# Kernel optimization log

Hardware: AMD Instinct MI355X
Metric: run time of the kernel (lower is better)

## Reference

```python
import jax, jax.numpy as jnp
import numpy as np

EMBED_DIM = 1024
BATCH, SEQ = 4, 2048


def setup_inputs() -> dict:
    key = jax.random.key(0)
    kx, kq, kk, kv = jax.random.split(key, 4)
    return {
        "x": jax.random.normal(kx, (BATCH, SEQ, EMBED_DIM), dtype=jnp.float32),
        "q_weight": jax.random.normal(kq, (EMBED_DIM, EMBED_DIM), dtype=jnp.float32),
        "k_weight": jax.random.normal(kk, (EMBED_DIM, EMBED_DIM), dtype=jnp.float32),
        "v_weight": jax.random.normal(kv, (EMBED_DIM, EMBED_DIM), dtype=jnp.float32),
    }


def reference(x, q_weight, k_weight, v_weight):
    # x: [b, s, d]
    d = x.shape[-1]
    Q = jnp.einsum('bsd,de->bse', x, q_weight)
    K = jnp.einsum('bsd,de->bse', x, k_weight)
    V = jnp.einsum('bsd,de->bse', x, v_weight)
    scores = jnp.einsum('bqe,bke->bqk', Q, K) / jnp.sqrt(jnp.float32(d))
    attn = jax.nn.softmax(scores, axis=-1)
    out = jnp.einsum('bqk,bke->bqe', attn, V)
    return out
```

## Files before the change

### kernel.cpp

```cpp
#include <hip/hip_runtime.h>
#include <hip/hip_bf16.h>


typedef _Float16 half8 __attribute__((ext_vector_type(8)));
typedef _Float16 half4v __attribute__((ext_vector_type(4)));
typedef float f32x16 __attribute__((ext_vector_type(16)));
typedef float f32x4 __attribute__((ext_vector_type(4)));

#define GLOBAL_AS __attribute__((address_space(1)))
#define LDS_AS __attribute__((address_space(3)))

__device__ __forceinline__ void gll16(const _Float16* g, _Float16* l) {
    __builtin_amdgcn_global_load_lds((GLOBAL_AS const void*)g, (LDS_AS void*)l, 16, 0, 0);
}

__device__ __forceinline__ void lgkm0_pin() {
    asm volatile("s_waitcnt lgkmcnt(0)" ::: "memory");
    __builtin_amdgcn_sched_barrier(0);
}

__device__ __forceinline__ void barrier_fence() {
    asm volatile("s_barrier" ::: "memory");
}

__device__ __forceinline__ void vmwait0() {
    asm volatile("s_waitcnt vmcnt(0)" ::: "memory");
}

__device__ __forceinline__ void vmwait4() {
    asm volatile("s_waitcnt vmcnt(4)" ::: "memory");
}

template <int NPROD, int OUTMODE>
__global__ __launch_bounds__(256) void gemm_nt(
    const _Float16* __restrict__ A0, const _Float16* __restrict__ A1,
    const _Float16* __restrict__ B0, const _Float16* __restrict__ B1,
    float* __restrict__ Cf, _Float16* __restrict__ C0, _Float16* __restrict__ C1,
    int lda, int ldb, int ldc, int K,
    long sA, long sB, long sC, float scale, float scale2) {
    constexpr int NTILES = (NPROD == 3) ? 4 : 2;
    constexpr int BUFH = NTILES * 4096;
    __shared__ alignas(16) _Float16 smem[2 * BUFH];

    const int tid = threadIdx.x;
    const int wave = tid >> 6, lane = tid & 63;
    const int wm = (wave >> 1) * 64, wn = (wave & 1) * 64;
    const int q2 = lane >> 5, r32 = lane & 31;

    const long zA = (long)blockIdx.z * sA;
    const long zB = (long)blockIdx.z * sB;
    const long zC = (long)blockIdx.z * sC;

    const float sc = (blockIdx.y * 2 < gridDim.y) ? scale : scale2;

    const int trow = tid >> 2;
    const int tcol = (((tid & 3) - ((tid >> 3) & 3) - ((tid >> 6) & 3)) & 3) * 8;
    const _Float16* gA0 = A0 + zA + (long)(blockIdx.x * 128 + trow) * lda + tcol;
    const _Float16* gB0 = B0 + zB + (long)(blockIdx.y * 128 + trow) * ldb + tcol;
    const _Float16* gA1 = (NPROD == 3) ? (A1 + zA + (long)(blockIdx.x * 128 + trow) * lda + tcol) : nullptr;
    const _Float16* gB1 = (NPROD == 3) ? (B1 + zB + (long)(blockIdx.y * 128 + trow) * ldb + tcol) : nullptr;

    f32x16 acc[2][2];
#pragma unroll
    for (int i = 0; i < 2; ++i)
#pragma unroll
        for (int j = 0; j < 2; ++j)
#pragma unroll
            for (int r = 0; r < 16; ++r) acc[i][j][r] = 0.f;

    const int ldsoff = tid * 8;
    const int fbase = q2 + (r32 >> 1) + (r32 >> 4);

    {
        _Float16* s = smem;
        gll16(gA0, s + ldsoff);
        gll16(gA0 + 64 * lda, s + ldsoff + 2048);
        gll16(gB0, s + 4096 + ldsoff);
        gll16(gB0 + 64 * ldb, s + 4096 + ldsoff + 2048);
        if (NPROD == 3) {
            gll16(gA1, s + 8192 + ldsoff);
            gll16(gA1 + 64 * lda, s + 8192 + ldsoff + 2048);
            gll16(gB1, s + 12288 + ldsoff);
            gll16(gB1 + 64 * ldb, s + 12288 + ldsoff + 2048);
        }
        gA0 += 32; gB0 += 32;
        if (NPROD == 3) { gA1 += 32; gB1 += 32; }
    }

    int buf = 0;
    for (int k0 = 0; k0 < K; k0 += 32) {
        __syncthreads();

        if (k0 + 32 < K) {
            _Float16* s = smem + (buf ^ 1) * BUFH;
            gll16(gA0, s + ldsoff);
            gll16(gA0 + 64 * lda, s + ldsoff + 2048);
            gll16(gB0, s + 4096 + ldsoff);
            gll16(gB0 + 64 * ldb, s + 4096 + ldsoff + 2048);
            if (NPROD == 3) {
                gll16(gA1, s + 8192 + ldsoff);
                gll16(gA1 + 64 * lda, s + 8192 + ldsoff + 2048);
                gll16(gB1, s + 12288 + ldsoff);
                gll16(gB1 + 64 * ldb, s + 12288 + ldsoff + 2048);
            }
            gA0 += 32; gB0 += 32;
            if (NPROD == 3) { gA1 += 32; gB1 += 32; }
        }

        _Float16* sA0 = smem + buf * BUFH;
        _Float16* sB0 = sA0 + 4096;
        _Float16* sA1 = (NPROD == 3) ? sA0 + 8192 : sA0;
        _Float16* sB1 = (NPROD == 3) ? sA0 + 12288 : sA0;
#pragma unroll
        for (int h = 0; h < 2; ++h) {
            half8 a0[2], b0[2], a1[2], b1[2];
#pragma unroll
            for (int i = 0; i < 2; ++i) {
                const int pp = ((fbase + 2 * i + 2 * h) & 3) * 8;
                a0[i] = *(const half8*)(sA0 + (wm + i * 32 + r32) * 32 + pp);
                b0[i] = *(const half8*)(sB0 + (wn + i * 32 + r32) * 32 + pp);
                if (NPROD == 3) {
                    a1[i] = *(const half8*)(sA1 + (wm + i * 32 + r32) * 32 + pp);
                    b1[i] = *(const half8*)(sB1 + (wn + i * 32 + r32) * 32 + pp);
                }
            }
#pragma unroll
            for (int i = 0; i < 2; ++i)
#pragma unroll
                for (int j = 0; j < 2; ++j) {
                    acc[i][j] = __builtin_amdgcn_mfma_f32_32x32x16_f16(a0[i], b0[j], acc[i][j], 0, 0, 0);
                    if (NPROD == 3) {
                        acc[i][j] = __builtin_amdgcn_mfma_f32_32x32x16_f16(a0[i], b1[j], acc[i][j], 0, 0, 0);
                        acc[i][j] = __builtin_amdgcn_mfma_f32_32x32x16_f16(a1[i], b0[j], acc[i][j], 0, 0, 0);
                    }
                }
        }
        buf ^= 1;
    }

    const int crow0 = blockIdx.x * 128 + wm + 4 * q2;
    const int ccol0 = blockIdx.y * 128 + wn + r32;
#pragma unroll
    for (int i = 0; i < 2; ++i)
#pragma unroll
        for (int j = 0; j < 2; ++j)
#pragma unroll
            for (int r = 0; r < 16; ++r) {
                int row = crow0 + i * 32 + (r & 3) + 8 * (r >> 2);
                long off = zC + (long)row * ldc + (ccol0 + j * 32);
                float v = acc[i][j][r] * sc;
                if (OUTMODE == 0) {
                    Cf[off] = v;
                } else if (OUTMODE == 2) {
                    C0[off] = (_Float16)v;
                } else {
                    _Float16 h = (_Float16)v;
                    C0[off] = h;
                    C1[off] = (_Float16)(v - (float)h);
                }
            }
}

__device__ __forceinline__ int frag_off(int fb, int lrow, int lc) {
    return (fb + lrow) * 32 + ((((fb >> 4) + lc + (lrow >> 1)) & 3) << 3);
}

__device__ __forceinline__ void ld4(half8 (&d)[4], const _Float16* base, int fb0,
                                    int lrow, int lc) {
#pragma unroll
    for (int f = 0; f < 4; ++f)
        d[f] = *(const half8*)(base + frag_off(fb0 + 16 * f, lrow, lc));
}

template <int MH>
__device__ __forceinline__ void mm16(f32x4 (&acc)[8][4], const half8 (&a)[4],
                                     const half8 (&b)[4]) {
#pragma unroll
    for (int i = 0; i < 4; ++i)
#pragma unroll
        for (int j = 0; j < 4; ++j)
            acc[MH * 4 + i][j] =
                __builtin_amdgcn_mfma_f32_16x16x32_f16(a[i], b[j], acc[MH * 4 + i][j], 0, 0, 0);
}

__device__ __forceinline__ void stage_tile(_Float16* dst, const _Float16* g, int ld,
                                           int ldsoff) {
    gll16(g, dst + ldsoff);
    gll16(g + (long)128 * ld, dst + 4096 + ldsoff);
}

template <int OUTMODE>
__global__ __launch_bounds__(512, 2) void gemm5p(
    const _Float16* __restrict__ A0, const _Float16* __restrict__ A1,
    const _Float16* __restrict__ B0, const _Float16* __restrict__ B1,
    float* __restrict__ Cf, _Float16* __restrict__ C0, _Float16* __restrict__ C1,
    int lda, int ldb, int ldc, int K,
    long sA, long sB, long sC, float scale, float scale2) {
    __shared__ alignas(16) _Float16 smem[65536];

    const int tid = threadIdx.x;
    const int wave = tid >> 6, lane = tid & 63;
    const int wm = (wave >> 2) * 128, wn = (wave & 3) * 64;
    const int lrow = lane & 15, lc = lane >> 4;

    const long zA = (long)blockIdx.z * sA;
    const long zB = (long)blockIdx.z * sB;
    const long zC = (long)blockIdx.z * sC;
    const float sc = (blockIdx.y * 2 < gridDim.y) ? scale : scale2;

    const int trow = tid >> 2;
    const int tcol = (((tid & 3) - ((tid >> 3) & 3) - ((tid >> 6) & 3)) & 3) * 8;
    const _Float16* gA0 = A0 + zA + (long)(blockIdx.x * 256 + trow) * lda + tcol;
    const _Float16* gB0 = B0 + zB + (long)(blockIdx.y * 256 + trow) * ldb + tcol;
    const _Float16* gA1 = A1 + zA + (long)(blockIdx.x * 256 + trow) * lda + tcol;
    const _Float16* gB1 = B1 + zB + (long)(blockIdx.y * 256 + trow) * ldb + tcol;

    const int ldsoff = tid * 8;

    f32x4 acc[8][4];
#pragma unroll
    for (int i = 0; i < 8; ++i)
#pragma unroll
        for (int j = 0; j < 4; ++j)
#pragma unroll
            for (int r = 0; r < 4; ++r) acc[i][j][r] = 0.f;

    const int nT = K >> 5;

    {
        _Float16* s = smem;
        stage_tile(s + 0, gA0, lda, ldsoff);
        stage_tile(s + 8192, gB0, ldb, ldsoff);
        stage_tile(s + 16384, gA1, lda, ldsoff);
        stage_tile(s + 24576, gB1, ldb, ldsoff);
        gA0 += 32; gB0 += 32; gA1 += 32; gB1 += 32;
        vmwait4();
        barrier_fence();
    }

    int buf = 0;
    for (int t = 0; t < nT; ++t) {
        _Float16* scur = smem + buf * 32768;
        _Float16* snx = smem + (buf ^ 1) * 32768;
        const bool pre = (t + 1 < nT);

        half8 a0L[4], a0H[4], a1L[4], a1H[4], b0[4], b1[4];

        ld4(a0L, scur, wm, lrow, lc);
        ld4(b0, scur + 8192, wn, lrow, lc);
        ld4(a0H, scur, wm + 64, lrow, lc);
        if (pre) {
            stage_tile(snx + 0, gA0, lda, ldsoff); gA0 += 32;
            stage_tile(snx + 8192, gB0, ldb, ldsoff); gB0 += 32;
        }
        __builtin_amdgcn_s_setprio(1);
        mm16<0>(acc, a0L, b0);
        mm16<1>(acc, a0H, b0);
        __builtin_amdgcn_s_setprio(0);
        if (pre) vmwait4();
        else vmwait0();
        barrier_fence();

        ld4(b1, scur + 24576, wn, lrow, lc);
        ld4(a1L, scur + 16384, wm, lrow, lc);
        ld4(a1H, scur + 16384, wm + 64, lrow, lc);
        if (pre) {
            stage_tile(snx + 16384, gA1, lda, ldsoff); gA1 += 32;
            stage_tile(snx + 24576, gB1, ldb, ldsoff); gB1 += 32;
        }
        __builtin_amdgcn_s_setprio(1);
        mm16<1>(acc, a0H, b1);
        mm16<0>(acc, a0L, b1);
        mm16<0>(acc, a1L, b0);
        mm16<1>(acc, a1H, b0);
        __builtin_amdgcn_s_setprio(0);
        if (pre) {
            lgkm0_pin();
            vmwait4();
            barrier_fence();
        }

        buf ^= 1;
    }

    const int crow0 = blockIdx.x * 256 + wm + lc * 4;
    const int ccol0 = blockIdx.y * 256 + wn + lrow;
#pragma unroll
    for (int mf = 0; mf < 8; ++mf)
#pragma unroll
        for (int nf = 0; nf < 4; ++nf)
#pragma unroll
            for (int r = 0; r < 4; ++r) {
                int row = crow0 + mf * 16 + r;
                long off = zC + (long)row * ldc + (ccol0 + nf * 16);
                float v = acc[mf][nf][r] * sc;
                if (OUTMODE == 0) {
                    Cf[off] = v;
                } else {
                    _Float16 h = (_Float16)v;
                    C0[off] = h;
                    C1[off] = (_Float16)(v - (float)h);
                }
            }
}

__global__ __launch_bounds__(256) void prep_fused(
    const float* __restrict__ x, _Float16* __restrict__ x0, _Float16* __restrict__ x1,
    long n4, int nsplit,
    const float* __restrict__ wq, const float* __restrict__ wk,
    const float* __restrict__ wv,
    _Float16* __restrict__ qk0, _Float16* __restrict__ qk1,
    _Float16* __restrict__ v0, _Float16* __restrict__ v1) {
    __shared__ float t[32][33];
    if ((int)blockIdx.x < nsplit) {
        long i = (long)blockIdx.x * 256 + threadIdx.x;
        if (i >= n4) return;
        float4 v = ((const float4*)x)[i];
        float a[4] = {v.x, v.y, v.z, v.w};
        half4v h, l;
#pragma unroll
        for (int c = 0; c < 4; ++c) {
            h[c] = (_Float16)a[c];
            l[c] = (_Float16)(a[c] - (float)h[c]);
        }
        ((half4v*)x0)[i] = h;
        ((half4v*)x1)[i] = l;
        return;
    }
    const int idx = blockIdx.x - nsplit;
    const int z = idx >> 10;
    const int tile = idx & 1023;
    const float* in = (z == 0) ? wq : (z == 1) ? wk : wv;
    _Float16* o0 = (z == 0) ? qk0 : (z == 1) ? qk0 + 1024 * 1024 : v0;
    _Float16* o1 = (z == 0) ? qk1 : (z == 1) ? qk1 + 1024 * 1024 : v1;

    const int c0 = (tile & 31) * 32, r0 = (tile >> 5) * 32;
    const int tx = threadIdx.x & 31, ty = threadIdx.x >> 5;
#pragma unroll
    for (int i = 0; i < 32; i += 8)
        t[ty + i][tx] = in[(long)(r0 + ty + i) * 1024 + c0 + tx];
    __syncthreads();
#pragma unroll
    for (int i = 0; i < 32; i += 8) {
        float v = t[tx][ty + i];
        _Float16 h = (_Float16)v;
        long o = (long)(c0 + ty + i) * 1024 + r0 + tx;
        o0[o] = h;
        o1[o] = (_Float16)(v - (float)h);
    }
}

__global__ __launch_bounds__(256) void softmax_rows(const float* __restrict__ S,
                                                    _Float16* __restrict__ P) {
    const int n = 2048;
    const long base = (long)blockIdx.x * n;
    const float4* row4 = (const float4*)(S + base);
    const int tid = threadIdx.x;
    const int wave = tid >> 6;

    float4 v0 = row4[tid * 2];
    float4 v1 = row4[tid * 2 + 1];
    float v[8] = {v0.x, v0.y, v0.z, v0.w, v1.x, v1.y, v1.z, v1.w};
    float lm = -3.4e38f;
#pragma unroll
    for (int t = 0; t < 8; ++t) lm = fmaxf(lm, v[t]);
#pragma unroll
    for (int o = 32; o > 0; o >>= 1) lm = fmaxf(lm, __shfl_xor(lm, o));
    __shared__ float redm[4];
    __shared__ float reds[4];
    if ((tid & 63) == 0) redm[wave] = lm;
    __syncthreads();
    lm = fmaxf(fmaxf(redm[0], redm[1]), fmaxf(redm[2], redm[3]));

    float e[8];
    float ls = 0.f;
#pragma unroll
    for (int t = 0; t < 8; ++t) {
        e[t] = __expf(v[t] - lm);
        ls += e[t];
    }
#pragma unroll
    for (int o = 32; o > 0; o >>= 1) ls += __shfl_xor(ls, o);
    if ((tid & 63) == 0) reds[wave] = ls;
    __syncthreads();
    ls = reds[0] + reds[1] + reds[2] + reds[3];
    const float inv = 1.f / ls;
    half8 p;
#pragma unroll
    for (int t = 0; t < 8; ++t) p[t] = (_Float16)(e[t] * inv);
    ((half8*)(P + base))[tid] = p;
}

extern "C" void kernel_launch(void* const* d_in, const int* in_sizes, int n_in,
                              void* d_out, int out_size, void* d_ws, size_t ws_size,
                              hipStream_t stream) {
    (void)in_sizes; (void)n_in; (void)out_size; (void)ws_size;
    const float* x = (const float*)d_in[0];
    const float* wq = (const float*)d_in[1];
    const float* wk = (const float*)d_in[2];
    const float* wv = (const float*)d_in[3];
    float* out = (float*)d_out;
    char* ws = (char*)d_ws;

    const long MB = 1l << 20;
    _Float16* Wqk0 = (_Float16*)(ws + 0 * MB);
    _Float16* Wqk1 = (_Float16*)(ws + 4 * MB);
    _Float16* Wv0  = (_Float16*)(ws + 8 * MB);
    _Float16* Wv1  = (_Float16*)(ws + 10 * MB);
    _Float16* x0   = (_Float16*)(ws + 12 * MB);
    _Float16* x1   = (_Float16*)(ws + 28 * MB);
    _Float16* P    = (_Float16*)(ws + 12 * MB);
    _Float16* QK0  = (_Float16*)(ws + 44 * MB);
    _Float16* QK1  = (_Float16*)(ws + 76 * MB);
    _Float16* Vt   = (_Float16*)(ws + 108 * MB);
    float*    S    = (float*)(ws + 124 * MB);

    const int B = 4, SEQ = 2048, D = 1024;
    const long M = (long)B * SEQ;
    const long ssq = (long)SEQ * SEQ;
    const int nsplit = (int)((M * D / 4 + 255) / 256);

    prep_fused<<<dim3(nsplit + 3072), dim3(256), 0, stream>>>(
        x, x0, x1, M * D / 4, nsplit, wq, wk, wv, Wqk0, Wqk1, Wv0, Wv1);

    gemm5p<1><<<dim3(32, 8, 1), dim3(512), 0, stream>>>(
        x0, x1, Wqk0, Wqk1, nullptr, QK0, QK1, D, D, 2 * D, D,
        0, 0, 0, 0.03125f, 1.0f);

    gemm_nt<1, 2><<<dim3(8, 64, 1), dim3(256), 0, stream>>>(
        Wv0, nullptr, x0, nullptr, nullptr, Vt, nullptr, D, D, (int)M, D,
        0, 0, 0, 1.0f, 1.0f);

    gemm5p<0><<<dim3(8, 8, B), dim3(512), 0, stream>>>(
        QK0, QK1, QK0 + D, QK1 + D, S, nullptr, nullptr, 2 * D, 2 * D, SEQ, D,
        (long)SEQ * 2 * D, (long)SEQ * 2 * D, ssq, 1.0f, 1.0f);

    softmax_rows<<<dim3(B * SEQ), dim3(256), 0, stream>>>(S, P);

    gemm_nt<1, 0><<<dim3(16, 8, B), dim3(256), 0, stream>>>(
        P, nullptr, Vt, nullptr, out, nullptr, nullptr, SEQ, (int)M, D, SEQ,
        ssq, (long)SEQ, (long)SEQ * D, 1.0f, 1.0f);
}
```

Before: 359.1 us.

## Fuse softmax into PV GEMM using row-max atomics from the score GEMM

The score GEMM epilogue now computes per-row maxima and publishes them through order-preserving uint atomicMax into a small buffer, which the prep kernel zeroes. A new pv_fused kernel reads fp32 scores directly, applies exp(s - max) while staging the A tile into LDS, accumulates row sums, and divides the output by the sum at the end. This removes the separate softmax pass and the fp16 P round trip through memory. It also drops the unused low-half V weight split. The cost is redundant exp work per N-tile (8 column blocks each recompute it) and wider fp32 reads of S inside the GEMM loop.

```diff
diff --git a/kernel.cpp b/kernel.cpp
--- a/kernel.cpp
+++ b/kernel.cpp
@@ -29,6 +29,15 @@
 
 __device__ __forceinline__ void vmwait4() {
     asm volatile("s_waitcnt vmcnt(4)" ::: "memory");
+}
+
+__device__ __forceinline__ unsigned encf(float f) {
+    unsigned b = __float_as_uint(f);
+    return (b & 0x80000000u) ? ~b : (b | 0x80000000u);
+}
+__device__ __forceinline__ float decf(unsigned u) {
+    unsigned b = (u & 0x80000000u) ? (u & 0x7FFFFFFFu) : ~u;
+    return __uint_as_float(b);
 }
 
 template <int NPROD, int OUTMODE>
@@ -194,6 +203,7 @@
     const _Float16* __restrict__ A0, const _Float16* __restrict__ A1,
     const _Float16* __restrict__ B0, const _Float16* __restrict__ B1,
     float* __restrict__ Cf, _Float16* __restrict__ C0, _Float16* __restrict__ C1,
+    unsigned* __restrict__ rmax,
     int lda, int ldb, int ldc, int K,
     long sA, long sB, long sC, float scale, float scale2) {
     __shared__ alignas(16) _Float16 smem[65536];
@@ -302,16 +312,160 @@
                     C1[off] = (_Float16)(v - (float)h);
                 }
             }
+
+    if constexpr (OUTMODE == 0) {
+#pragma unroll
+        for (int mf = 0; mf < 8; ++mf)
+#pragma unroll
+            for (int r = 0; r < 4; ++r) {
+                float v = fmaxf(fmaxf(acc[mf][0][r], acc[mf][1][r]),
+                                fmaxf(acc[mf][2][r], acc[mf][3][r]));
+                v = fmaxf(v, __shfl_xor(v, 1));
+                v = fmaxf(v, __shfl_xor(v, 2));
+                v = fmaxf(v, __shfl_xor(v, 4));
+                v = fmaxf(v, __shfl_xor(v, 8));
+                if (lrow == 0) {
+                    int rl = blockIdx.x * 256 + wm + lc * 4 + mf * 16 + r;
+                    atomicMax(rmax + (long)blockIdx.z * 2048 + rl, encf(v * sc));
+                }
+            }
+    }
+}
+
+__device__ __forceinline__ void pv_loadS(const float* gS, int k0, int cc0, int cc1,
+                                         float4& s0, float4& s1, float4& s2, float4& s3) {
+    s0 = *(const float4*)(gS + k0 + cc0 * 8);
+    s1 = *(const float4*)(gS + k0 + cc0 * 8 + 4);
+    s2 = *(const float4*)(gS + k0 + cc1 * 8);
+    s3 = *(const float4*)(gS + k0 + cc1 * 8 + 4);
+}
+
+__device__ __forceinline__ void pv_writeA(_Float16* dst, int arow, int p0, int p1,
+                                          float mrow, float& lacc,
+                                          const float4& s0, const float4& s1,
+                                          const float4& s2, const float4& s3) {
+    float e[16] = {s0.x, s0.y, s0.z, s0.w, s1.x, s1.y, s1.z, s1.w,
+                   s2.x, s2.y, s2.z, s2.w, s3.x, s3.y, s3.z, s3.w};
+    half8 h0, h1;
+#pragma unroll
+    for (int j = 0; j < 8; ++j) {
+        float v0 = __expf(e[j] - mrow);
+        float v1 = __expf(e[j + 8] - mrow);
+        lacc += v0 + v1;
+        h0[j] = (_Float16)v0;
+        h1[j] = (_Float16)v1;
+    }
+    *(half8*)(dst + arow * 32 + p0 * 8) = h0;
+    *(half8*)(dst + arow * 32 + p1 * 8) = h1;
+}
+
+__global__ __launch_bounds__(256) void pv_fused(
+    const float* __restrict__ S, const unsigned* __restrict__ rmax,
+    const _Float16* __restrict__ Vt, float* __restrict__ out) {
+    constexpr int BUFH = 8192;
+    __shared__ alignas(16) _Float16 smem[2 * BUFH];
+
+    const int tid = threadIdx.x;
+    const int wave = tid >> 6, lane = tid & 63;
+    const int wm = (wave >> 1) * 64, wn = (wave & 1) * 64;
+    const int q2 = lane >> 5, r32 = lane & 31;
+    const int bz = blockIdx.z;
+
+    const int arow = tid >> 1;
+    const int fA = ((arow >> 1) + (arow >> 4)) & 3;
+    const int p0 = 2 * (tid & 1), p1 = p0 + 1;
+    const int cc0 = (p0 - fA) & 3, cc1 = (p1 - fA) & 3;
+    const float* gS = S + (long)bz * 2048 * 2048 + (long)(blockIdx.x * 128 + arow) * 2048;
+    const float mrow = decf(rmax[bz * 2048 + blockIdx.x * 128 + arow]);
+
+    const int trow = tid >> 2;
+    const int tcol = (((tid & 3) - ((tid >> 3) & 3) - ((tid >> 6) & 3)) & 3) * 8;
+    const _Float16* gB = Vt + (long)(blockIdx.y * 128 + trow) * 8192 + (long)bz * 2048 + tcol;
+
+    const int ldsoff = tid * 8;
+    const int fbase = q2 + (r32 >> 1) + (r32 >> 4);
+
+    f32x16 acc[2][2];
+#pragma unroll
+    for (int i = 0; i < 2; ++i)
+#pragma unroll
+        for (int j = 0; j < 2; ++j)
+#pragma unroll
+            for (int r = 0; r < 16; ++r) acc[i][j][r] = 0.f;
+
+    float lacc = 0.f;
+    float4 s0, s1, s2, s3;
+
+    pv_loadS(gS, 0, cc0, cc1, s0, s1, s2, s3);
+    gll16(gB, smem + 4096 + ldsoff);
+    gll16(gB + 64 * 8192, smem + 4096 + ldsoff + 2048);
+    gB += 32;
+    pv_writeA(smem, arow, p0, p1, mrow, lacc, s0, s1, s2, s3);
+    __syncthreads();
+
+    int buf = 0;
+    for (int t = 0; t < 64; ++t) {
+        const bool pre = (t + 1 < 64);
+        _Float16* scur = smem + buf * BUFH;
+        _Float16* snx = smem + (buf ^ 1) * BUFH;
+
+        if (pre) {
+            pv_loadS(gS, (t + 1) * 32, cc0, cc1, s0, s1, s2, s3);
+            gll16(gB, snx + 4096 + ldsoff);
+            gll16(gB + 64 * 8192, snx + 4096 + ldsoff + 2048);
+            gB += 32;
+        }
+
+        _Float16* sB = scur + 4096;
+#pragma unroll
+        for (int h = 0; h < 2; ++h) {
+            half8 a0[2], b0[2];
+#pragma unroll
+            for (int i = 0; i < 2; ++i) {
+                const int pp = ((fbase + 2 * i + 2 * h) & 3) * 8;
+                a0[i] = *(const half8*)(scur + (wm + i * 32 + r32) * 32 + pp);
+                b0[i] = *(const half8*)(sB + (wn + i * 32 + r32) * 32 + pp);
+            }
+#pragma unroll
+            for (int i = 0; i < 2; ++i)
+#pragma unroll
+                for (int j = 0; j < 2; ++j)
+                    acc[i][j] = __builtin_amdgcn_mfma_f32_32x32x16_f16(a0[i], b0[j], acc[i][j], 0, 0, 0);
+        }
+
+        if (pre) pv_writeA(snx, arow, p0, p1, mrow, lacc, s0, s1, s2, s3);
+        __syncthreads();
+        buf ^= 1;
+    }
+
+    float* lbuf = (float*)smem;
+    lbuf[tid] = lacc;
+    __syncthreads();
+
+    const int ccol0 = blockIdx.y * 128 + wn + r32;
+#pragma unroll
+    for (int i = 0; i < 2; ++i)
+#pragma unroll
+        for (int j = 0; j < 2; ++j)
+#pragma unroll
+            for (int r = 0; r < 16; ++r) {
+                int rl = wm + 4 * q2 + i * 32 + (r & 3) + 8 * (r >> 2);
+                float l = lbuf[2 * rl] + lbuf[2 * rl + 1];
+                int row = blockIdx.x * 128 + rl;
+                long off = (long)bz * 2048 * 1024 + (long)row * 1024 + (ccol0 + j * 32);
+                out[off] = acc[i][j][r] / l;
+            }
 }
 
 __global__ __launch_bounds__(256) void prep_fused(
     const float* __restrict__ x, _Float16* __restrict__ x0, _Float16* __restrict__ x1,
-    long n4, int nsplit,
+    long n4, int nsplit, unsigned* __restrict__ rmax,
     const float* __restrict__ wq, const float* __restrict__ wk,
     const float* __restrict__ wv,
     _Float16* __restrict__ qk0, _Float16* __restrict__ qk1,
-    _Float16* __restrict__ v0, _Float16* __restrict__ v1) {
+    _Float16* __restrict__ v0) {
     __shared__ float t[32][33];
+    if ((int)blockIdx.x < 32) rmax[blockIdx.x * 256 + threadIdx.x] = 0u;
     if ((int)blockIdx.x < nsplit) {
         long i = (long)blockIdx.x * 256 + threadIdx.x;
         if (i >= n4) return;
@@ -332,7 +486,7 @@
     const int tile = idx & 1023;
     const float* in = (z == 0) ? wq : (z == 1) ? wk : wv;
     _Float16* o0 = (z == 0) ? qk0 : (z == 1) ? qk0 + 1024 * 1024 : v0;
-    _Float16* o1 = (z == 0) ? qk1 : (z == 1) ? qk1 + 1024 * 1024 : v1;
+    _Float16* o1 = (z == 0) ? qk1 : qk1 + 1024 * 1024;
 
     const int c0 = (tile & 31) * 32, r0 = (tile >> 5) * 32;
     const int tx = threadIdx.x & 31, ty = threadIdx.x >> 5;
@@ -346,49 +500,8 @@
         _Float16 h = (_Float16)v;
         long o = (long)(c0 + ty + i) * 1024 + r0 + tx;
         o0[o] = h;
-        o1[o] = (_Float16)(v - (float)h);
-    }
-}
-
-__global__ __launch_bounds__(256) void softmax_rows(const float* __restrict__ S,
-                                                    _Float16* __restrict__ P) {
-    const int n = 2048;
-    const long base = (long)blockIdx.x * n;
-    const float4* row4 = (const float4*)(S + base);
-    const int tid = threadIdx.x;
-    const int wave = tid >> 6;
-
-    float4 v0 = row4[tid * 2];
-    float4 v1 = row4[tid * 2 + 1];
-    float v[8] = {v0.x, v0.y, v0.z, v0.w, v1.x, v1.y, v1.z, v1.w};
-    float lm = -3.4e38f;
-#pragma unroll
-    for (int t = 0; t < 8; ++t) lm = fmaxf(lm, v[t]);
-#pragma unroll
-    for (int o = 32; o > 0; o >>= 1) lm = fmaxf(lm, __shfl_xor(lm, o));
-    __shared__ float redm[4];
-    __shared__ float reds[4];
-    if ((tid & 63) == 0) redm[wave] = lm;
-    __syncthreads();
-    lm = fmaxf(fmaxf(redm[0], redm[1]), fmaxf(redm[2], redm[3]));
-
-    float e[8];
-    float ls = 0.f;
-#pragma unroll
-    for (int t = 0; t < 8; ++t) {
-        e[t] = __expf(v[t] - lm);
-        ls += e[t];
-    }
-#pragma unroll
-    for (int o = 32; o > 0; o >>= 1) ls += __shfl_xor(ls, o);
-    if ((tid & 63) == 0) reds[wave] = ls;
-    __syncthreads();
-    ls = reds[0] + reds[1] + reds[2] + reds[3];
-    const float inv = 1.f / ls;
-    half8 p;
-#pragma unroll
-    for (int t = 0; t < 8; ++t) p[t] = (_Float16)(e[t] * inv);
-    ((half8*)(P + base))[tid] = p;
+        if (z < 2) o1[o] = (_Float16)(v - (float)h);
+    }
 }
 
 extern "C" void kernel_launch(void* const* d_in, const int* in_sizes, int n_in,
@@ -406,10 +519,9 @@
     _Float16* Wqk0 = (_Float16*)(ws + 0 * MB);
     _Float16* Wqk1 = (_Float16*)(ws + 4 * MB);
     _Float16* Wv0  = (_Float16*)(ws + 8 * MB);
-    _Float16* Wv1  = (_Float16*)(ws + 10 * MB);
+    unsigned* rmax = (unsigned*)(ws + 10 * MB);
     _Float16* x0   = (_Float16*)(ws + 12 * MB);
     _Float16* x1   = (_Float16*)(ws + 28 * MB);
-    _Float16* P    = (_Float16*)(ws + 12 * MB);
     _Float16* QK0  = (_Float16*)(ws + 44 * MB);
     _Float16* QK1  = (_Float16*)(ws + 76 * MB);
     _Float16* Vt   = (_Float16*)(ws + 108 * MB);
@@ -421,10 +533,10 @@
     const int nsplit = (int)((M * D / 4 + 255) / 256);
 
     prep_fused<<<dim3(nsplit + 3072), dim3(256), 0, stream>>>(
-        x, x0, x1, M * D / 4, nsplit, wq, wk, wv, Wqk0, Wqk1, Wv0, Wv1);
+        x, x0, x1, M * D / 4, nsplit, rmax, wq, wk, wv, Wqk0, Wqk1, Wv0);
 
     gemm5p<1><<<dim3(32, 8, 1), dim3(512), 0, stream>>>(
-        x0, x1, Wqk0, Wqk1, nullptr, QK0, QK1, D, D, 2 * D, D,
+        x0, x1, Wqk0, Wqk1, nullptr, QK0, QK1, nullptr, D, D, 2 * D, D,
         0, 0, 0, 0.03125f, 1.0f);
 
     gemm_nt<1, 2><<<dim3(8, 64, 1), dim3(256), 0, stream>>>(
@@ -432,12 +544,8 @@
         0, 0, 0, 1.0f, 1.0f);
 
     gemm5p<0><<<dim3(8, 8, B), dim3(512), 0, stream>>>(
-        QK0, QK1, QK0 + D, QK1 + D, S, nullptr, nullptr, 2 * D, 2 * D, SEQ, D,
+        QK0, QK1, QK0 + D, QK1 + D, S, nullptr, nullptr, rmax, 2 * D, 2 * D, SEQ, D,
         (long)SEQ * 2 * D, (long)SEQ * 2 * D, ssq, 1.0f, 1.0f);
 
-    softmax_rows<<<dim3(B * SEQ), dim3(256), 0, stream>>>(S, P);
-
-    gemm_nt<1, 0><<<dim3(16, 8, B), dim3(256), 0, stream>>>(
-        P, nullptr, Vt, nullptr, out, nullptr, nullptr, SEQ, (int)M, D, SEQ,
-        ssq, (long)SEQ, (long)SEQ * D, 1.0f, 1.0f);
-}
+    pv_fused<<<dim3(16, 8, B), dim3(256), 0, stream>>>(S, rmax, Vt, out);
+}
```

Measured after the change: 387.1 us. +7.8%, slower.

## Add dedicated 256x128 double-buffered PV GEMM kernel and drop unused Wv low split

Applied to the files above, without the earlier changes.

Replaces the generic gemm_nt launch for P·V with a specialized 512-thread kernel. Each block computes a 256x128 output tile, double-buffers LDS via global_load_lds, raises wave priority around its MFMA blocks and uses 2-block occupancy launch bounds. This aims to increase data reuse per block and to overlap loads with MFMA compared with the previous 128-row tiles. The prep kernel also stops writing the unused low-half fp16 split of Wv, which removes some wasted memory writes.

```diff
diff --git a/kernel.cpp b/kernel.cpp
--- a/kernel.cpp
+++ b/kernel.cpp
@@ -304,13 +304,96 @@
             }
 }
 
+__global__ __launch_bounds__(512, 2) void pv2(
+    const _Float16* __restrict__ P, const _Float16* __restrict__ Vt,
+    float* __restrict__ out) {
+    constexpr int ABUF = 8192;
+    constexpr int BUFH = ABUF + 4096;
+    __shared__ alignas(16) _Float16 smem[2 * BUFH];
+
+    const int tid = threadIdx.x;
+    const int wave = tid >> 6, lane = tid & 63;
+    const int wm = (wave >> 2) * 128, wn = (wave & 3) * 32;
+    const int lrow = lane & 15, lc = lane >> 4;
+    const int bz = blockIdx.z;
+
+    const int trow = tid >> 2;
+    const int tcol = (((tid & 3) - ((tid >> 3) & 3) - ((tid >> 6) & 3)) & 3) * 8;
+    const _Float16* gA = P + (long)(bz * 2048 + blockIdx.x * 256 + trow) * 2048 + tcol;
+    const _Float16* gB = Vt + (long)(blockIdx.y * 128 + trow) * 8192 + bz * 2048 + tcol;
+
+    const int ldsoff = tid * 8;
+
+    f32x4 acc[8][2];
+#pragma unroll
+    for (int i = 0; i < 8; ++i)
+#pragma unroll
+        for (int j = 0; j < 2; ++j)
+#pragma unroll
+            for (int r = 0; r < 4; ++r) acc[i][j][r] = 0.f;
+
+    gll16(gA, smem + ldsoff);
+    gll16(gA + (long)128 * 2048, smem + 4096 + ldsoff);
+    gll16(gB, smem + ABUF + ldsoff);
+    gA += 32; gB += 32;
+    vmwait0();
+    barrier_fence();
+
+    int buf = 0;
+    for (int t = 0; t < 64; ++t) {
+        _Float16* scur = smem + buf * BUFH;
+        _Float16* snx = smem + (buf ^ 1) * BUFH;
+        const bool pre = (t + 1 < 64);
+
+        half8 aL[4], aH[4], b[2];
+        ld4(aL, scur, wm, lrow, lc);
+        ld4(aH, scur, wm + 64, lrow, lc);
+        b[0] = *(const half8*)(scur + ABUF + frag_off(wn, lrow, lc));
+        b[1] = *(const half8*)(scur + ABUF + frag_off(wn + 16, lrow, lc));
+        if (pre) {
+            gll16(gA, snx + ldsoff);
+            gll16(gA + (long)128 * 2048, snx + 4096 + ldsoff);
+            gll16(gB, snx + ABUF + ldsoff);
+            gA += 32; gB += 32;
+        }
+        __builtin_amdgcn_s_setprio(1);
+#pragma unroll
+        for (int i = 0; i < 4; ++i)
+#pragma unroll
+            for (int j = 0; j < 2; ++j) {
+                acc[i][j] = __builtin_amdgcn_mfma_f32_16x16x32_f16(aL[i], b[j], acc[i][j], 0, 0, 0);
+                acc[4 + i][j] = __builtin_amdgcn_mfma_f32_16x16x32_f16(aH[i], b[j], acc[4 + i][j], 0, 0, 0);
+            }
+        __builtin_amdgcn_s_setprio(0);
+        if (pre) {
+            lgkm0_pin();
+            vmwait0();
+            barrier_fence();
+        }
+        buf ^= 1;
+    }
+
+    const int crow0 = blockIdx.x * 256 + wm + lc * 4;
+    const int ccol0 = blockIdx.y * 128 + wn + lrow;
+#pragma unroll
+    for (int mf = 0; mf < 8; ++mf)
+#pragma unroll
+        for (int nj = 0; nj < 2; ++nj)
+#pragma unroll
+            for (int r = 0; r < 4; ++r) {
+                int row = crow0 + mf * 16 + r;
+                long off = (long)bz * 2048 * 1024 + (long)row * 1024 + (ccol0 + nj * 16);
+                out[off] = acc[mf][nj][r];
+            }
+}
+
 __global__ __launch_bounds__(256) void prep_fused(
     const float* __restrict__ x, _Float16* __restrict__ x0, _Float16* __restrict__ x1,
     long n4, int nsplit,
     const float* __restrict__ wq, const float* __restrict__ wk,
     const float* __restrict__ wv,
     _Float16* __restrict__ qk0, _Float16* __restrict__ qk1,
-    _Float16* __restrict__ v0, _Float16* __restrict__ v1) {
+    _Float16* __restrict__ v0) {
     __shared__ float t[32][33];
     if ((int)blockIdx.x < nsplit) {
         long i = (long)blockIdx.x * 256 + threadIdx.x;
@@ -332,7 +415,7 @@
     const int tile = idx & 1023;
     const float* in = (z == 0) ? wq : (z == 1) ? wk : wv;
     _Float16* o0 = (z == 0) ? qk0 : (z == 1) ? qk0 + 1024 * 1024 : v0;
-    _Float16* o1 = (z == 0) ? qk1 : (z == 1) ? qk1 + 1024 * 1024 : v1;
+    _Float16* o1 = (z == 0) ? qk1 : qk1 + 1024 * 1024;
 
     const int c0 = (tile & 31) * 32, r0 = (tile >> 5) * 32;
     const int tx = threadIdx.x & 31, ty = threadIdx.x >> 5;
@@ -346,7 +429,7 @@
         _Float16 h = (_Float16)v;
         long o = (long)(c0 + ty + i) * 1024 + r0 + tx;
         o0[o] = h;
-        o1[o] = (_Float16)(v - (float)h);
+        if (z < 2) o1[o] = (_Float16)(v - (float)h);
     }
 }
 
@@ -406,7 +489,6 @@
     _Float16* Wqk0 = (_Float16*)(ws + 0 * MB);
     _Float16* Wqk1 = (_Float16*)(ws + 4 * MB);
     _Float16* Wv0  = (_Float16*)(ws + 8 * MB);
-    _Float16* Wv1  = (_Float16*)(ws + 10 * MB);
     _Float16* x0   = (_Float16*)(ws + 12 * MB);
     _Float16* x1   = (_Float16*)(ws + 28 * MB);
     _Float16* P    = (_Float16*)(ws + 12 * MB);
@@ -421,7 +503,7 @@
     const int nsplit = (int)((M * D / 4 + 255) / 256);
 
     prep_fused<<<dim3(nsplit + 3072), dim3(256), 0, stream>>>(
-        x, x0, x1, M * D / 4, nsplit, wq, wk, wv, Wqk0, Wqk1, Wv0, Wv1);
+        x, x0, x1, M * D / 4, nsplit, wq, wk, wv, Wqk0, Wqk1, Wv0);
 
     gemm5p<1><<<dim3(32, 8, 1), dim3(512), 0, stream>>>(
         x0, x1, Wqk0, Wqk1, nullptr, QK0, QK1, D, D, 2 * D, D,
@@ -437,7 +519,5 @@
 
     softmax_rows<<<dim3(B * SEQ), dim3(256), 0, stream>>>(S, P);
 
-    gemm_nt<1, 0><<<dim3(16, 8, B), dim3(256), 0, stream>>>(
-        P, nullptr, Vt, nullptr, out, nullptr, nullptr, SEQ, (int)M, D, SEQ,
-        ssq, (long)SEQ, (long)SEQ * D, 1.0f, 1.0f);
-}
+    pv2<<<dim3(8, 8, B), dim3(512), 0, stream>>>(P, Vt, out);
+}
```

Result: no change. 364.9 us (+1.6%).

## Add 256x128-tile split-fp16 GEMM for QK^T scores and drop unused Wv low half

Applied to the files above, without the earlier changes.

Adds a new gemm2b kernel with a 256x128 block tile and 8x2 MFMA fragments per wave, computing the three split-fp16 product terms (hi*hi, hi*lo, lo*hi). It replaces gemm5p for the Q·K^T score GEMM and doubles the grid in the N dimension. The intent is to raise occupancy or parallelism and change the load balance of the score GEMM. Separately, prep_fused stops writing the low-half residual of Wv, since only Wv0 was consumed, which saves global writes. The new kernel loads synchronously with no double buffering, so memory latency may be exposed.

```diff
diff --git a/kernel.cpp b/kernel.cpp
--- a/kernel.cpp
+++ b/kernel.cpp
@@ -304,13 +304,117 @@
             }
 }
 
+template <int OUTMODE>
+__global__ __launch_bounds__(512) void gemm2b(
+    const _Float16* __restrict__ A0, const _Float16* __restrict__ A1,
+    const _Float16* __restrict__ B0, const _Float16* __restrict__ B1,
+    float* __restrict__ Cf, _Float16* __restrict__ C0, _Float16* __restrict__ C1,
+    int lda, int ldb, int ldc, int K,
+    long sA, long sB, long sC, float scale, float scale2) {
+    __shared__ alignas(16) _Float16 smem[24576];
+
+    const int tid = threadIdx.x;
+    const int wave = tid >> 6, lane = tid & 63;
+    const int wm = (wave >> 2) * 128, wn = (wave & 3) * 32;
+    const int lrow = lane & 15, lc = lane >> 4;
+
+    const long zA = (long)blockIdx.z * sA;
+    const long zB = (long)blockIdx.z * sB;
+    const long zC = (long)blockIdx.z * sC;
+    const float sc = (blockIdx.y * 2 < gridDim.y) ? scale : scale2;
+
+    const int trow = tid >> 2;
+    const int tcol = (((tid & 3) - ((tid >> 3) & 3) - ((tid >> 6) & 3)) & 3) * 8;
+    const _Float16* gA0 = A0 + zA + (long)(blockIdx.x * 256 + trow) * lda + tcol;
+    const _Float16* gB0 = B0 + zB + (long)(blockIdx.y * 128 + trow) * ldb + tcol;
+    const _Float16* gA1 = A1 + zA + (long)(blockIdx.x * 256 + trow) * lda + tcol;
+    const _Float16* gB1 = B1 + zB + (long)(blockIdx.y * 128 + trow) * ldb + tcol;
+
+    const int ldsoff = tid * 8;
+
+    f32x4 acc[8][2];
+#pragma unroll
+    for (int i = 0; i < 8; ++i)
+#pragma unroll
+        for (int j = 0; j < 2; ++j)
+#pragma unroll
+            for (int r = 0; r < 4; ++r) acc[i][j][r] = 0.f;
+
+    const int nT = K >> 5;
+
+    for (int t = 0; t < nT; ++t) {
+        gll16(gA0, smem + ldsoff);
+        gll16(gA0 + 128 * lda, smem + 4096 + ldsoff);
+        gll16(gB0, smem + 8192 + ldsoff);
+        gll16(gA1, smem + 12288 + ldsoff);
+        gll16(gA1 + 128 * lda, smem + 16384 + ldsoff);
+        gll16(gB1, smem + 20480 + ldsoff);
+        gA0 += 32; gB0 += 32; gA1 += 32; gB1 += 32;
+        vmwait0();
+        barrier_fence();
+
+        half8 a[8], b0f[2], b1f[2];
+#pragma unroll
+        for (int m = 0; m < 8; ++m)
+            a[m] = *(const half8*)(smem + frag_off(wm + 16 * m, lrow, lc));
+        b0f[0] = *(const half8*)(smem + 8192 + frag_off(wn, lrow, lc));
+        b0f[1] = *(const half8*)(smem + 8192 + frag_off(wn + 16, lrow, lc));
+        b1f[0] = *(const half8*)(smem + 20480 + frag_off(wn, lrow, lc));
+        b1f[1] = *(const half8*)(smem + 20480 + frag_off(wn + 16, lrow, lc));
+        __builtin_amdgcn_s_setprio(1);
+#pragma unroll
+        for (int m = 0; m < 8; ++m)
+#pragma unroll
+            for (int n = 0; n < 2; ++n)
+                acc[m][n] = __builtin_amdgcn_mfma_f32_16x16x32_f16(a[m], b0f[n], acc[m][n], 0, 0, 0);
+#pragma unroll
+        for (int m = 0; m < 8; ++m)
+#pragma unroll
+            for (int n = 0; n < 2; ++n)
+                acc[m][n] = __builtin_amdgcn_mfma_f32_16x16x32_f16(a[m], b1f[n], acc[m][n], 0, 0, 0);
+        __builtin_amdgcn_s_setprio(0);
+#pragma unroll
+        for (int m = 0; m < 8; ++m)
+            a[m] = *(const half8*)(smem + 12288 + frag_off(wm + 16 * m, lrow, lc));
+        __builtin_amdgcn_s_setprio(1);
+#pragma unroll
+        for (int m = 0; m < 8; ++m)
+#pragma unroll
+            for (int n = 0; n < 2; ++n)
+                acc[m][n] = __builtin_amdgcn_mfma_f32_16x16x32_f16(a[m], b0f[n], acc[m][n], 0, 0, 0);
+        __builtin_amdgcn_s_setprio(0);
+        lgkm0_pin();
+        barrier_fence();
+    }
+
+    const int crow0 = blockIdx.x * 256 + wm + lc * 4;
+    const int ccol0 = blockIdx.y * 128 + wn + lrow;
+#pragma unroll
+    for (int mf = 0; mf < 8; ++mf)
+#pragma unroll
+        for (int nf = 0; nf < 2; ++nf)
+#pragma unroll
+            for (int r = 0; r < 4; ++r) {
+                int row = crow0 + mf * 16 + r;
+                long off = zC + (long)row * ldc + (ccol0 + nf * 16);
+                float v = acc[mf][nf][r] * sc;
+                if (OUTMODE == 0) {
+                    Cf[off] = v;
+                } else {
+                    _Float16 h = (_Float16)v;
+                    C0[off] = h;
+                    C1[off] = (_Float16)(v - (float)h);
+                }
+            }
+}
+
 __global__ __launch_bounds__(256) void prep_fused(
     const float* __restrict__ x, _Float16* __restrict__ x0, _Float16* __restrict__ x1,
     long n4, int nsplit,
     const float* __restrict__ wq, const float* __restrict__ wk,
     const float* __restrict__ wv,
     _Float16* __restrict__ qk0, _Float16* __restrict__ qk1,
-    _Float16* __restrict__ v0, _Float16* __restrict__ v1) {
+    _Float16* __restrict__ v0) {
     __shared__ float t[32][33];
     if ((int)blockIdx.x < nsplit) {
         long i = (long)blockIdx.x * 256 + threadIdx.x;
@@ -332,7 +436,7 @@
     const int tile = idx & 1023;
     const float* in = (z == 0) ? wq : (z == 1) ? wk : wv;
     _Float16* o0 = (z == 0) ? qk0 : (z == 1) ? qk0 + 1024 * 1024 : v0;
-    _Float16* o1 = (z == 0) ? qk1 : (z == 1) ? qk1 + 1024 * 1024 : v1;
+    _Float16* o1 = (z == 0) ? qk1 : qk1 + 1024 * 1024;
 
     const int c0 = (tile & 31) * 32, r0 = (tile >> 5) * 32;
     const int tx = threadIdx.x & 31, ty = threadIdx.x >> 5;
@@ -346,7 +450,7 @@
         _Float16 h = (_Float16)v;
         long o = (long)(c0 + ty + i) * 1024 + r0 + tx;
         o0[o] = h;
-        o1[o] = (_Float16)(v - (float)h);
+        if (z < 2) o1[o] = (_Float16)(v - (float)h);
     }
 }
 
@@ -406,7 +510,6 @@
     _Float16* Wqk0 = (_Float16*)(ws + 0 * MB);
     _Float16* Wqk1 = (_Float16*)(ws + 4 * MB);
     _Float16* Wv0  = (_Float16*)(ws + 8 * MB);
-    _Float16* Wv1  = (_Float16*)(ws + 10 * MB);
     _Float16* x0   = (_Float16*)(ws + 12 * MB);
     _Float16* x1   = (_Float16*)(ws + 28 * MB);
     _Float16* P    = (_Float16*)(ws + 12 * MB);
@@ -421,7 +524,7 @@
     const int nsplit = (int)((M * D / 4 + 255) / 256);
 
     prep_fused<<<dim3(nsplit + 3072), dim3(256), 0, stream>>>(
-        x, x0, x1, M * D / 4, nsplit, wq, wk, wv, Wqk0, Wqk1, Wv0, Wv1);
+        x, x0, x1, M * D / 4, nsplit, wq, wk, wv, Wqk0, Wqk1, Wv0);
 
     gemm5p<1><<<dim3(32, 8, 1), dim3(512), 0, stream>>>(
         x0, x1, Wqk0, Wqk1, nullptr, QK0, QK1, D, D, 2 * D, D,
@@ -431,7 +534,7 @@
         Wv0, nullptr, x0, nullptr, nullptr, Vt, nullptr, D, D, (int)M, D,
         0, 0, 0, 1.0f, 1.0f);
 
-    gemm5p<0><<<dim3(8, 8, B), dim3(512), 0, stream>>>(
+    gemm2b<0><<<dim3(8, 16, B), dim3(512), 0, stream>>>(
         QK0, QK1, QK0 + D, QK1 + D, S, nullptr, nullptr, 2 * D, 2 * D, SEQ, D,
         (long)SEQ * 2 * D, (long)SEQ * 2 * D, ssq, 1.0f, 1.0f);
 
```

After: 383.5 us. +6.8%, slower.
